# Kernel optimization log

Measured on AMD Instinct MI355X. Metric: run time of the kernel, lower is better.

Reference implementation:

```python
import jax, jax.numpy as jnp
import numpy as np

N = 20000
E = 320000
NODE_DIM = 9
EDGE_DIM = 4
HID = 64
EHID = 32  # hidden_dim // 2, edge feature dim inside GAT layers
HEADS = 4
OUT_DIM = 256
NUM_LAYERS = 3


def layer_norm(x, g, b, eps=1e-5):
    m = jnp.mean(x, axis=-1, keepdims=True)
    v = jnp.mean((x - m) ** 2, axis=-1, keepdims=True)
    return (x - m) / jnp.sqrt(v + eps) * g + b


def setup_inputs():
    key = jax.random.key(0)
    ks = iter(jax.random.split(key, 48))
    def w(shape, scale=0.1):
        return jax.random.normal(next(ks), shape, dtype=jnp.float32) * scale
    inp = {
        "x": jax.random.normal(next(ks), (N, NODE_DIM), dtype=jnp.float32),
        "edge_attr": jax.random.normal(next(ks), (E, EDGE_DIM), dtype=jnp.float32),
        "edge_index": jax.random.randint(next(ks), (2, E), 0, N, dtype=jnp.int32),
        # node encoder: Linear(9,32)+ReLU+Linear(32,64)+LayerNorm(64)
        "ne_w1": w((NODE_DIM, 32)), "ne_b1": jnp.zeros((32,), jnp.float32),
        "ne_w2": w((32, HID)), "ne_b2": jnp.zeros((HID,), jnp.float32),
        "ne_g": jnp.ones((HID,), jnp.float32), "ne_beta": jnp.zeros((HID,), jnp.float32),
        # edge encoder: Linear(4,16)+ReLU+Linear(16,32)+LayerNorm(32)
        "ee_w1": w((EDGE_DIM, 16)), "ee_b1": jnp.zeros((16,), jnp.float32),
        "ee_w2": w((16, EHID)), "ee_b2": jnp.zeros((EHID,), jnp.float32),
        "ee_g": jnp.ones((EHID,), jnp.float32), "ee_beta": jnp.zeros((EHID,), jnp.float32),
        # risk attention: Linear(96,64)+Tanh+Linear(64,1)+Sigmoid
        "ra_w1": w((HID + EHID, HID)), "ra_b1": jnp.zeros((HID,), jnp.float32),
        "ra_w2": w((HID, 1)), "ra_b2": jnp.zeros((1,), jnp.float32),
        # GAT layers (stacked over NUM_LAYERS; identical shapes)
        "gat_wl": w((NUM_LAYERS, HID, HEADS * HID)),       # linear (no bias)
        "gat_wa": w((NUM_LAYERS, 2 * HID + EHID)),          # attention (out=1, no bias)
        "gat_we": w((NUM_LAYERS, EHID, HEADS * HID)),       # edge_transform (no bias)
        "gat_wo": w((NUM_LAYERS, HID, HID)),                # output_transform weight
        "gat_wob": jnp.zeros((NUM_LAYERS, HID), jnp.float32),
        # output layer: Linear(64,128)+ReLU+Linear(128,256)+LayerNorm(256)
        "ow_1": w((HID, 128)), "ob_1": jnp.zeros((128,), jnp.float32),
        "ow_2": w((128, OUT_DIM)), "ob_2": jnp.zeros((OUT_DIM,), jnp.float32),
        "o_g": jnp.ones((OUT_DIM,), jnp.float32), "o_beta": jnp.zeros((OUT_DIM,), jnp.float32),
    }
    return inp


def reference(x, edge_attr, edge_index,
              ne_w1, ne_b1, ne_w2, ne_b2, ne_g, ne_beta,
              ee_w1, ee_b1, ee_w2, ee_b2, ee_g, ee_beta,
              ra_w1, ra_b1, ra_w2, ra_b2,
              gat_wl, gat_wa, gat_we, gat_wo, gat_wob,
              ow_1, ob_1, ow_2, ob_2, o_g, o_beta):
    row, col = edge_index[0], edge_index[1]
    # encoders
    h = layer_norm(jax.nn.relu(x @ ne_w1 + ne_b1) @ ne_w2 + ne_b2, ne_g, ne_beta)            # [N, 64]
    ef = layer_norm(jax.nn.relu(edge_attr @ ee_w1 + ee_b1) @ ee_w2 + ee_b2, ee_g, ee_beta)   # [E, 32]
    # risk weights per edge
    ri = jnp.concatenate([h[row], ef], axis=1)                                                # [E, 96]
    rw = jax.nn.sigmoid(jnp.tanh(ri @ ra_w1 + ra_b1) @ ra_w2 + ra_b2)                         # [E, 1]
    xh = h
    for l in range(NUM_LAYERS):
        xproj = (xh @ gat_wl[l]).reshape(N, HEADS, HID)                                       # [N, H, 64]
        emsg = (ef @ gat_we[l]).reshape(E, HEADS, HID)                                        # [E, H, 64]
        # attention Linear(2*64+32 -> 1) split into three slices; avoids materializing the
        # [E, H, 160] concat. Same math: cat([x_i, x_j, ef]) @ wa.
        wa_i = gat_wa[l][:HID]
        wa_j = gat_wa[l][HID:2 * HID]
        wa_e = gat_wa[l][2 * HID:]
        x_j = xproj[col]                                                                      # [E, H, 64]
        alpha = xproj[row] @ wa_i + x_j @ wa_j + (ef @ wa_e)[:, None]                         # [E, H]
        alpha = jnp.where(alpha >= 0, alpha, 0.2 * alpha)  # leaky_relu(0.2)
        alpha = alpha * rw                                  # risk modulation (broadcast [E,1])
        alpha = jax.nn.softmax(alpha, axis=0)               # softmax over ALL edges per head (as in torch code)
        agg = jax.ops.segment_sum(alpha[:, :, None] * (x_j + emsg), col, num_segments=N)      # [N, H, 64]
        xh = jax.nn.relu(agg.mean(axis=1) @ gat_wo[l] + gat_wob[l])                           # [N, 64]
    out = layer_norm(jax.nn.relu(xh @ ow_1 + ob_1) @ ow_2 + ob_2, o_g, o_beta)                # [N, 256]
    return out
```

## Files before the change

kernel.cpp:

```cpp
#include <hip/hip_runtime.h>
#include <math.h>

#define NN 20000
#define EE 320000
#define HID 64
#define EHID 32
#define HEADS 4

__device__ __forceinline__ float fast_tanh(float x) {
  float e = __expf(2.f * x);
  return 1.f - 2.f * __builtin_amdgcn_rcpf(e + 1.f);
}
__device__ __forceinline__ float fast_sigmoid(float x) {
  return __builtin_amdgcn_rcpf(1.f + __expf(-x));
}
__device__ __forceinline__ float bcast8(float v, int q) {
  switch (q) {
    case 0: return __int_as_float(__builtin_amdgcn_ds_swizzle(__float_as_int(v), (0 << 5) | 0x18));
    case 1: return __int_as_float(__builtin_amdgcn_ds_swizzle(__float_as_int(v), (1 << 5) | 0x18));
    case 2: return __int_as_float(__builtin_amdgcn_ds_swizzle(__float_as_int(v), (2 << 5) | 0x18));
    case 3: return __int_as_float(__builtin_amdgcn_ds_swizzle(__float_as_int(v), (3 << 5) | 0x18));
    case 4: return __int_as_float(__builtin_amdgcn_ds_swizzle(__float_as_int(v), (4 << 5) | 0x18));
    case 5: return __int_as_float(__builtin_amdgcn_ds_swizzle(__float_as_int(v), (5 << 5) | 0x18));
    case 6: return __int_as_float(__builtin_amdgcn_ds_swizzle(__float_as_int(v), (6 << 5) | 0x18));
    default: return __int_as_float(__builtin_amdgcn_ds_swizzle(__float_as_int(v), (7 << 5) | 0x18));
  }
}

__global__ __launch_bounds__(256) void k_node_enc(
    const float* __restrict__ x, const float* __restrict__ w1, const float* __restrict__ b1,
    const float* __restrict__ w2, const float* __restrict__ b2,
    const float* __restrict__ g, const float* __restrict__ beta,
    float* __restrict__ h) {
  int n = blockIdx.x * blockDim.x + threadIdx.x;
  if (n >= NN) return;
  float xin[9];
#pragma unroll
  for (int k = 0; k < 9; k++) xin[k] = x[n * 9 + k];
  float hid[32];
#pragma unroll
  for (int j = 0; j < 32; j++) {
    float a = b1[j];
#pragma unroll
    for (int k = 0; k < 9; k++) a += xin[k] * w1[k * 32 + j];
    hid[j] = fmaxf(a, 0.f);
  }
  float o[64];
  float s = 0.f;
  for (int j = 0; j < 64; j++) {
    float a = b2[j];
#pragma unroll
    for (int k = 0; k < 32; k++) a += hid[k] * w2[k * 64 + j];
    o[j] = a;
    s += a;
  }
  float m = s * (1.f / 64.f);
  float v = 0.f;
  for (int j = 0; j < 64; j++) { float d = o[j] - m; v += d * d; }
  v *= (1.f / 64.f);
  float inv = rsqrtf(v + 1e-5f);
#pragma unroll
  for (int j4 = 0; j4 < 16; j4++) {
    float4 r;
    r.x = (o[j4 * 4 + 0] - m) * inv * g[j4 * 4 + 0] + beta[j4 * 4 + 0];
    r.y = (o[j4 * 4 + 1] - m) * inv * g[j4 * 4 + 1] + beta[j4 * 4 + 1];
    r.z = (o[j4 * 4 + 2] - m) * inv * g[j4 * 4 + 2] + beta[j4 * 4 + 2];
    r.w = (o[j4 * 4 + 3] - m) * inv * g[j4 * 4 + 3] + beta[j4 * 4 + 3];
    ((float4*)&h[n * 64])[j4] = r;
  }
}

__global__ __launch_bounds__(256) void k_hist(const int* __restrict__ ei, int* __restrict__ counts) {
  int e = blockIdx.x * 256 + threadIdx.x;
  if (e < EE) atomicAdd(&counts[ei[EE + e]], 1);
}
__global__ __launch_bounds__(1024) void k_scan(
    const int* __restrict__ counts, int* __restrict__ rowptr, int* __restrict__ cursor) {
  __shared__ int wsum[16];
  int t = threadIdx.x, lane = t & 63, w = t >> 6;
  const int CH = 20;
  int base_i = t * CH;
  int local = 0;
  for (int i = 0; i < CH; i++) {
    int idx = base_i + i;
    if (idx < NN) local += counts[idx];
  }
  int v = local;
#pragma unroll
  for (int off = 1; off < 64; off <<= 1) {
    int u = __shfl_up(v, off);
    if (lane >= off) v += u;
  }
  if (lane == 63) wsum[w] = v;
  __syncthreads();
  int wbase = 0;
  for (int i = 0; i < w; i++) wbase += wsum[i];
  int run = wbase + v - local;
  for (int i = 0; i < CH; i++) {
    int idx = base_i + i;
    if (idx < NN) {
      rowptr[idx] = run;
      cursor[idx] = run;
      run += counts[idx];
    }
  }
  if (t == 1023) rowptr[NN] = EE;
}

__global__ __launch_bounds__(256) void k_edge_enc(
    const float* __restrict__ ea, const float* __restrict__ w1, const float* __restrict__ b1,
    const float* __restrict__ w2, const float* __restrict__ b2,
    const float* __restrict__ g, const float* __restrict__ beta,
    const float* __restrict__ gat_wa, const int* __restrict__ ei,
    int* __restrict__ cursor,
    float* __restrict__ efs, float4* __restrict__ devs4, int2* __restrict__ rcs) {
  int e = blockIdx.x * blockDim.x + threadIdx.x;
  if (e >= EE) return;
  int row = ei[e], col = ei[EE + e];
  int pos = atomicAdd(&cursor[col], 1);
  float4 xin = ((const float4*)ea)[e];
  float hid[16];
#pragma unroll
  for (int j = 0; j < 16; j++) {
    float a = b1[j];
    a += xin.x * w1[0 * 16 + j];
    a += xin.y * w1[1 * 16 + j];
    a += xin.z * w1[2 * 16 + j];
    a += xin.w * w1[3 * 16 + j];
    hid[j] = fmaxf(a, 0.f);
  }
  float o[32];
  float s = 0.f;
#pragma unroll
  for (int j = 0; j < 32; j++) {
    float a = b2[j];
#pragma unroll
    for (int k = 0; k < 16; k++) a += hid[k] * w2[k * 32 + j];
    o[j] = a;
    s += a;
  }
  float m = s * (1.f / 32.f);
  float v = 0.f;
#pragma unroll
  for (int j = 0; j < 32; j++) { float d = o[j] - m; v += d * d; }
  v *= (1.f / 32.f);
  float inv = rsqrtf(v + 1e-5f);
  float d0 = 0.f, d1 = 0.f, d2 = 0.f;
  float vn[32];
#pragma unroll
  for (int j = 0; j < 32; j++) {
    vn[j] = (o[j] - m) * inv * g[j] + beta[j];
    d0 += vn[j] * gat_wa[0 * 160 + 128 + j];
    d1 += vn[j] * gat_wa[1 * 160 + 128 + j];
    d2 += vn[j] * gat_wa[2 * 160 + 128 + j];
  }
#pragma unroll
  for (int j4 = 0; j4 < 8; j4++) {
    float4 r;
    r.x = vn[j4 * 4 + 0]; r.y = vn[j4 * 4 + 1]; r.z = vn[j4 * 4 + 2]; r.w = vn[j4 * 4 + 3];
    ((float4*)&efs[(size_t)pos * 32])[j4] = r;
  }
  devs4[pos] = make_float4(d0, d1, d2, 0.f);
  rcs[pos] = make_int2(row, col);
}

__global__ __launch_bounds__(256) void k_risk_node(
    const float* __restrict__ h, const float* __restrict__ w1, const float* __restrict__ b1,
    float* __restrict__ hnode) {
  __shared__ float xsT[64][20];
  int t = threadIdx.x;
  int n0 = blockIdx.x * 16;
  const float4* h4 = (const float4*)h;
  {
    int m = t & 15, k4 = t >> 4;
    float4 xv = h4[(n0 + m) * 16 + k4];
    xsT[k4 * 4 + 0][m] = xv.x;
    xsT[k4 * 4 + 1][m] = xv.y;
    xsT[k4 * 4 + 2][m] = xv.z;
    xsT[k4 * 4 + 3][m] = xv.w;
  }
  __syncthreads();
  int j = t & 63, grp = t >> 6;
  float bv = b1[j];
  float a0 = bv, a1 = bv, a2 = bv, a3 = bv;
  for (int k = 0; k < 64; k++) {
    float wv = w1[k * 64 + j];
    float4 xv = *(const float4*)&xsT[k][grp * 4];
    a0 += xv.x * wv; a1 += xv.y * wv; a2 += xv.z * wv; a3 += xv.w * wv;
  }
  hnode[(n0 + grp * 4 + 0) * 64 + j] = a0;
  hnode[(n0 + grp * 4 + 1) * 64 + j] = a1;
  hnode[(n0 + grp * 4 + 2) * 64 + j] = a2;
  hnode[(n0 + grp * 4 + 3) * 64 + j] = a3;
}

__global__ __launch_bounds__(256) void k_risk_edge(
    const float* __restrict__ hnode, const float* __restrict__ efs, const int2* __restrict__ rcs,
    const float* __restrict__ w1e, const float* __restrict__ w2, const float* __restrict__ b2_,
    float* __restrict__ rws) {
  int t = threadIdx.x, lane = t & 63;
  int s = lane & 7;
  int p = blockIdx.x * 256 + t;
  int myrow = rcs[p].x;
  const float4* hnode4 = (const float4*)hnode;
  const float4* efs4 = (const float4*)efs;
  const float4* w1e4 = (const float4*)w1e;
  const float4* w24 = (const float4*)w2;
  float ev[32];
#pragma unroll
  for (int i = 0; i < 8; i++) {
    float4 tmp = efs4[(size_t)p * 8 + i];
    ev[i * 4 + 0] = tmp.x; ev[i * 4 + 1] = tmp.y; ev[i * 4 + 2] = tmp.z; ev[i * 4 + 3] = tmp.w;
  }
  int rowq[8];
#pragma unroll
  for (int q = 0; q < 8; q++)
    rowq[q] = __float_as_int(bcast8(__int_as_float(myrow), q));
  float acc[8][8];
#pragma unroll
  for (int q = 0; q < 8; q++) {
    float4 ha = hnode4[(size_t)rowq[q] * 16 + s * 2];
    float4 hb = hnode4[(size_t)rowq[q] * 16 + s * 2 + 1];
    acc[q][0] = ha.x; acc[q][1] = ha.y; acc[q][2] = ha.z; acc[q][3] = ha.w;
    acc[q][4] = hb.x; acc[q][5] = hb.y; acc[q][6] = hb.z; acc[q][7] = hb.w;
  }
#pragma unroll
  for (int k = 0; k < 32; k++) {
    float4 wa4 = w1e4[k * 16 + s * 2];
    float4 wb4 = w1e4[k * 16 + s * 2 + 1];
#pragma unroll
    for (int q = 0; q < 8; q++) {
      float ekq = bcast8(ev[k], q);
      acc[q][0] += ekq * wa4.x; acc[q][1] += ekq * wa4.y;
      acc[q][2] += ekq * wa4.z; acc[q][3] += ekq * wa4.w;
      acc[q][4] += ekq * wb4.x; acc[q][5] += ekq * wb4.y;
      acc[q][6] += ekq * wb4.z; acc[q][7] += ekq * wb4.w;
    }
  }
  float4 wva = w24[s * 2], wvb = w24[s * 2 + 1];
  float tq[8];
#pragma unroll
  for (int q = 0; q < 8; q++) {
    tq[q] = fast_tanh(acc[q][0]) * wva.x + fast_tanh(acc[q][1]) * wva.y +
            fast_tanh(acc[q][2]) * wva.z + fast_tanh(acc[q][3]) * wva.w +
            fast_tanh(acc[q][4]) * wvb.x + fast_tanh(acc[q][5]) * wvb.y +
            fast_tanh(acc[q][6]) * wvb.z + fast_tanh(acc[q][7]) * wvb.w;
  }
#pragma unroll
  for (int q = 0; q < 8; q++) {
    tq[q] += __shfl_xor(tq[q], 1);
    tq[q] += __shfl_xor(tq[q], 2);
    tq[q] += __shfl_xor(tq[q], 4);
  }
  float mine = tq[0];
  mine = (s == 1) ? tq[1] : mine;
  mine = (s == 2) ? tq[2] : mine;
  mine = (s == 3) ? tq[3] : mine;
  mine = (s == 4) ? tq[4] : mine;
  mine = (s == 5) ? tq[5] : mine;
  mine = (s == 6) ? tq[6] : mine;
  mine = (s == 7) ? tq[7] : mine;
  rws[p] = fast_sigmoid(mine + b2_[0]);
}

__global__ __launch_bounds__(256) void k_xproj(
    const float* __restrict__ xh, const float* __restrict__ wl, const float* __restrict__ wa,
    float* __restrict__ xproj, float* __restrict__ di, float* __restrict__ dj) {
  __shared__ float xsT[64][20];
  int t = threadIdx.x, lane = t & 63, w = t >> 6;
  int n0 = blockIdx.x * 16;
  const float4* xh4 = (const float4*)xh;
  {
    int m = t & 15, k4 = t >> 4;
    float4 xv = xh4[(n0 + m) * 16 + k4];
    xsT[k4 * 4 + 0][m] = xv.x;
    xsT[k4 * 4 + 1][m] = xv.y;
    xsT[k4 * 4 + 2][m] = xv.z;
    xsT[k4 * 4 + 3][m] = xv.w;
  }
  __syncthreads();
  float acc[16];
#pragma unroll
  for (int m = 0; m < 16; m++) acc[m] = 0.f;
  for (int k = 0; k < 64; k++) {
    float wv = wl[k * 256 + t];
    float4 xa = *(const float4*)&xsT[k][0];
    float4 xb = *(const float4*)&xsT[k][4];
    float4 xc = *(const float4*)&xsT[k][8];
    float4 xd = *(const float4*)&xsT[k][12];
    acc[0] += xa.x * wv; acc[1] += xa.y * wv; acc[2] += xa.z * wv; acc[3] += xa.w * wv;
    acc[4] += xb.x * wv; acc[5] += xb.y * wv; acc[6] += xb.z * wv; acc[7] += xb.w * wv;
    acc[8] += xc.x * wv; acc[9] += xc.y * wv; acc[10] += xc.z * wv; acc[11] += xc.w * wv;
    acc[12] += xd.x * wv; acc[13] += xd.y * wv; acc[14] += xd.z * wv; acc[15] += xd.w * wv;
  }
  float wai = wa[lane], waj = wa[64 + lane];
#pragma unroll
  for (int m = 0; m < 16; m++) {
    xproj[(n0 + m) * 256 + t] = acc[m];
    float vi = acc[m] * wai;
    float vj = acc[m] * waj;
#pragma unroll
    for (int off = 32; off; off >>= 1) { vi += __shfl_xor(vi, off); vj += __shfl_xor(vj, off); }
    if (lane == 0) { di[(n0 + m) * 4 + w] = vi; dj[(n0 + m) * 4 + w] = vj; }
  }
}

__global__ __launch_bounds__(256) void k_pexp(
    const int2* __restrict__ rcs, const float4* __restrict__ devs4,
    const float* __restrict__ rws, const float* __restrict__ di,
    const float* __restrict__ dj, int layer,
    float4* __restrict__ ps4, float* __restrict__ gsum_l) {
  __shared__ float wred[4][4];
  int t = threadIdx.x, lane = t & 63, w = t >> 6;
  int i = blockIdx.x * 256 + t;
  int2 rc = rcs[i];
  float4 dv = devs4[i];
  float dev = (layer == 0) ? dv.x : ((layer == 1) ? dv.y : dv.z);
  float rv = rws[i];
  float4 dr = ((const float4*)di)[rc.x];
  float4 djc = ((const float4*)dj)[rc.y];
  float z0 = dr.x + djc.x + dev, z1 = dr.y + djc.y + dev;
  float z2 = dr.z + djc.z + dev, z3 = dr.w + djc.w + dev;
  z0 = ((z0 >= 0.f) ? z0 : 0.2f * z0) * rv;
  z1 = ((z1 >= 0.f) ? z1 : 0.2f * z1) * rv;
  z2 = ((z2 >= 0.f) ? z2 : 0.2f * z2) * rv;
  z3 = ((z3 >= 0.f) ? z3 : 0.2f * z3) * rv;
  float4 pv;
  pv.x = __expf(z0); pv.y = __expf(z1); pv.z = __expf(z2); pv.w = __expf(z3);
  ps4[i] = pv;
  float sh[4] = {pv.x, pv.y, pv.z, pv.w};
#pragma unroll
  for (int h = 0; h < 4; h++) {
    float v = sh[h];
#pragma unroll
    for (int off = 32; off; off >>= 1) v += __shfl_xor(v, off);
    if (lane == 0) wred[w][h] = v;
  }
  __syncthreads();
  if (t < 4) atomicAdd(&gsum_l[t], wred[0][t] + wred[1][t] + wred[2][t] + wred[3][t]);
}

__global__ __launch_bounds__(256) void k_agg(
    const int* __restrict__ rowptr, const float4* __restrict__ ps4,
    const float* __restrict__ efs,
    float* __restrict__ sagg, float* __restrict__ tagg) {
  int t = threadIdx.x, lane = t & 63, wv = t >> 6;
  int n = blockIdx.x * 4 + wv;
  int c = lane & 31, slot = lane >> 5;
  float a0 = 0.f, a1 = 0.f, a2 = 0.f, a3 = 0.f;
  float s0 = 0.f, s1 = 0.f, s2 = 0.f, s3 = 0.f;
  int beg = rowptr[n], end = rowptr[n + 1];
  int i = beg + slot;
  for (; i + 2 < end; i += 4) {
    float4 pa = ps4[i];
    float eva = efs[(size_t)i * 32 + c];
    float4 pb = ps4[i + 2];
    float evb = efs[(size_t)(i + 2) * 32 + c];
    a0 += pa.x * eva + pb.x * evb;
    a1 += pa.y * eva + pb.y * evb;
    a2 += pa.z * eva + pb.z * evb;
    a3 += pa.w * eva + pb.w * evb;
    s0 += pa.x + pb.x; s1 += pa.y + pb.y;
    s2 += pa.z + pb.z; s3 += pa.w + pb.w;
  }
  if (i < end) {
    float4 pa = ps4[i];
    float eva = efs[(size_t)i * 32 + c];
    a0 += pa.x * eva; a1 += pa.y * eva; a2 += pa.z * eva; a3 += pa.w * eva;
    s0 += pa.x; s1 += pa.y; s2 += pa.z; s3 += pa.w;
  }
  a0 += __shfl_xor(a0, 32); a1 += __shfl_xor(a1, 32);
  a2 += __shfl_xor(a2, 32); a3 += __shfl_xor(a3, 32);
  s0 += __shfl_xor(s0, 32); s1 += __shfl_xor(s1, 32);
  s2 += __shfl_xor(s2, 32); s3 += __shfl_xor(s3, 32);
  if (slot == 0) {
    tagg[n * 128 + 0 * 32 + c] = a0;
    tagg[n * 128 + 1 * 32 + c] = a1;
    tagg[n * 128 + 2 * 32 + c] = a2;
    tagg[n * 128 + 3 * 32 + c] = a3;
    if (c < 4) {
      float sv = (c == 0) ? s0 : (c == 1) ? s1 : (c == 2) ? s2 : s3;
      sagg[n * 4 + c] = sv;
    }
  }
}

template <bool DO_XPROJ>
__global__ __launch_bounds__(256) void k_update_fused(
    const float* __restrict__ xproj, const float* __restrict__ sagg,
    const float* __restrict__ tagg, const float* __restrict__ gsum_l,
    const float* __restrict__ we, const float* __restrict__ wo, const float* __restrict__ wob,
    const float* __restrict__ wl_next, const float* __restrict__ wa_next,
    float* __restrict__ xh_out, float* __restrict__ xproj_out,
    float* __restrict__ di, float* __restrict__ dj) {
  __shared__ float tsT[128][20];
  __shared__ float usT[64][20];
  __shared__ float xhT[64][20];
  __shared__ float ss[16][4];
  int t = threadIdx.x, lane = t & 63, w = t >> 6;
  int n0 = blockIdx.x * 16;
  float4 gs = *((const float4*)gsum_l);
  float inv0 = 1.0f / gs.x, inv1 = 1.0f / gs.y, inv2 = 1.0f / gs.z, inv3 = 1.0f / gs.w;
  const float4* tagg4 = (const float4*)tagg;
  for (int i = t; i < 16 * 32; i += 256) {
    int m = i & 15, k4 = i >> 4;
    float invh = (k4 < 8) ? inv0 : (k4 < 16) ? inv1 : (k4 < 24) ? inv2 : inv3;
    float4 tv = tagg4[(n0 + m) * 32 + k4];
    tsT[k4 * 4 + 0][m] = tv.x * invh;
    tsT[k4 * 4 + 1][m] = tv.y * invh;
    tsT[k4 * 4 + 2][m] = tv.z * invh;
    tsT[k4 * 4 + 3][m] = tv.w * invh;
  }
  if (t < 64) {
    int hh = t & 3;
    float invh = (hh == 0) ? inv0 : (hh == 1) ? inv1 : (hh == 2) ? inv2 : inv3;
    ss[t >> 2][hh] = sagg[n0 * 4 + t] * invh;
  }
  __syncthreads();
  int j = lane, grp = w;
  float u0 = 0.f, u1 = 0.f, u2 = 0.f, u3 = 0.f;
#pragma unroll
  for (int h = 0; h < 4; h++) {
    u0 += xproj[(n0 + grp * 4 + 0) * 256 + h * 64 + j] * ss[grp * 4 + 0][h];
    u1 += xproj[(n0 + grp * 4 + 1) * 256 + h * 64 + j] * ss[grp * 4 + 1][h];
    u2 += xproj[(n0 + grp * 4 + 2) * 256 + h * 64 + j] * ss[grp * 4 + 2][h];
    u3 += xproj[(n0 + grp * 4 + 3) * 256 + h * 64 + j] * ss[grp * 4 + 3][h];
  }
  for (int hc = 0; hc < 128; hc++) {
    float wv = we[(hc & 31) * 256 + (hc >> 5) * 64 + j];
    float4 tv = *(const float4*)&tsT[hc][grp * 4];
    u0 += tv.x * wv; u1 += tv.y * wv; u2 += tv.z * wv; u3 += tv.w * wv;
  }
  *(float4*)&usT[j][grp * 4] = make_float4(u0 * 0.25f, u1 * 0.25f, u2 * 0.25f, u3 * 0.25f);
  __syncthreads();
  float ob = wob[j];
  float o0 = ob, o1 = ob, o2 = ob, o3 = ob;
  for (int k = 0; k < 64; k++) {
    float wv = wo[k * 64 + j];
    float4 uv = *(const float4*)&usT[k][grp * 4];
    o0 += uv.x * wv; o1 += uv.y * wv; o2 += uv.z * wv; o3 += uv.w * wv;
  }
  o0 = fmaxf(o0, 0.f); o1 = fmaxf(o1, 0.f); o2 = fmaxf(o2, 0.f); o3 = fmaxf(o3, 0.f);
  if (!DO_XPROJ) {
    xh_out[(n0 + grp * 4 + 0) * 64 + j] = o0;
    xh_out[(n0 + grp * 4 + 1) * 64 + j] = o1;
    xh_out[(n0 + grp * 4 + 2) * 64 + j] = o2;
    xh_out[(n0 + grp * 4 + 3) * 64 + j] = o3;
    return;
  }
  xhT[j][grp * 4 + 0] = o0;
  xhT[j][grp * 4 + 1] = o1;
  xhT[j][grp * 4 + 2] = o2;
  xhT[j][grp * 4 + 3] = o3;
  __syncthreads();
  float acc[16];
#pragma unroll
  for (int m = 0; m < 16; m++) acc[m] = 0.f;
  for (int k = 0; k < 64; k++) {
    float wv = wl_next[k * 256 + t];
    float4 xa = *(const float4*)&xhT[k][0];
    float4 xb = *(const float4*)&xhT[k][4];
    float4 xc = *(const float4*)&xhT[k][8];
    float4 xd = *(const float4*)&xhT[k][12];
    acc[0] += xa.x * wv; acc[1] += xa.y * wv; acc[2] += xa.z * wv; acc[3] += xa.w * wv;
    acc[4] += xb.x * wv; acc[5] += xb.y * wv; acc[6] += xb.z * wv; acc[7] += xb.w * wv;
    acc[8] += xc.x * wv; acc[9] += xc.y * wv; acc[10] += xc.z * wv; acc[11] += xc.w * wv;
    acc[12] += xd.x * wv; acc[13] += xd.y * wv; acc[14] += xd.z * wv; acc[15] += xd.w * wv;
  }
  float wai = wa_next[lane], waj = wa_next[64 + lane];
#pragma unroll
  for (int m = 0; m < 16; m++) {
    xproj_out[(n0 + m) * 256 + t] = acc[m];
    float vi = acc[m] * wai;
    float vj = acc[m] * waj;
#pragma unroll
    for (int off = 32; off; off >>= 1) { vi += __shfl_xor(vi, off); vj += __shfl_xor(vj, off); }
    if (lane == 0) { di[(n0 + m) * 4 + w] = vi; dj[(n0 + m) * 4 + w] = vj; }
  }
}

#define OPN 8
__global__ __launch_bounds__(256) void k_out(
    const float* __restrict__ xh, const float* __restrict__ w1, const float* __restrict__ b1,
    const float* __restrict__ w2, const float* __restrict__ b2,
    const float* __restrict__ g, const float* __restrict__ beta,
    float* __restrict__ out) {
  __shared__ float xsT[64][12];
  __shared__ float hsT[128][12];
  __shared__ float wp[4], wq[4];
  int t = threadIdx.x, lane = t & 63, w = t >> 6;
  int n0 = blockIdx.x * OPN;
  const float4* xh4 = (const float4*)xh;
  if (t < 128) {
    int m = t >> 4, k4 = t & 15;
    float4 xv = xh4[(n0 + m) * 16 + k4];
    xsT[k4 * 4 + 0][m] = xv.x;
    xsT[k4 * 4 + 1][m] = xv.y;
    xsT[k4 * 4 + 2][m] = xv.z;
    xsT[k4 * 4 + 3][m] = xv.w;
  }
  __syncthreads();
  for (int i = t; i < OPN * 128; i += 256) {
    int m = i >> 7, jj = i & 127;
    float a = b1[jj];
#pragma unroll
    for (int k = 0; k < 64; k++) a += xsT[k][m] * w1[k * 128 + jj];
    hsT[jj][m] = fmaxf(a, 0.f);
  }
  __syncthreads();
  float o[OPN];
  float bb = b2[t];
#pragma unroll
  for (int m = 0; m < OPN; m++) o[m] = bb;
  for (int k = 0; k < 128; k++) {
    float wv = w2[k * 256 + t];
    float4 ha = *(const float4*)&hsT[k][0];
    float4 hb = *(const float4*)&hsT[k][4];
    o[0] += ha.x * wv; o[1] += ha.y * wv; o[2] += ha.z * wv; o[3] += ha.w * wv;
    o[4] += hb.x * wv; o[5] += hb.y * wv; o[6] += hb.z * wv; o[7] += hb.w * wv;
  }
  float gv = g[t], bv = beta[t];
#pragma unroll
  for (int m = 0; m < OPN; m++) {
    float v = o[m], vv = o[m] * o[m];
#pragma unroll
    for (int off = 32; off; off >>= 1) { v += __shfl_xor(v, off); vv += __shfl_xor(vv, off); }
    if (lane == 0) { wp[w] = v; wq[w] = vv; }
    __syncthreads();
    float mean = (wp[0] + wp[1] + wp[2] + wp[3]) * (1.f / 256.f);
    float ex2 = (wq[0] + wq[1] + wq[2] + wq[3]) * (1.f / 256.f);
    float var = ex2 - mean * mean;
    __syncthreads();
    out[(n0 + m) * 256 + t] = (o[m] - mean) * rsqrtf(var + 1e-5f) * gv + bv;
  }
}

extern "C" void kernel_launch(void* const* d_in, const int* in_sizes, int n_in,
                              void* d_out, int out_size, void* d_ws, size_t ws_size,
                              hipStream_t stream) {
  const float* x         = (const float*)d_in[0];
  const float* edge_attr = (const float*)d_in[1];
  const int*   ei        = (const int*)d_in[2];
  const float* ne_w1 = (const float*)d_in[3];
  const float* ne_b1 = (const float*)d_in[4];
  const float* ne_w2 = (const float*)d_in[5];
  const float* ne_b2 = (const float*)d_in[6];
  const float* ne_g  = (const float*)d_in[7];
  const float* ne_be = (const float*)d_in[8];
  const float* ee_w1 = (const float*)d_in[9];
  const float* ee_b1 = (const float*)d_in[10];
  const float* ee_w2 = (const float*)d_in[11];
  const float* ee_b2 = (const float*)d_in[12];
  const float* ee_g  = (const float*)d_in[13];
  const float* ee_be = (const float*)d_in[14];
  const float* ra_w1 = (const float*)d_in[15];
  const float* ra_b1 = (const float*)d_in[16];
  const float* ra_w2 = (const float*)d_in[17];
  const float* ra_b2 = (const float*)d_in[18];
  const float* gat_wl  = (const float*)d_in[19];
  const float* gat_wa  = (const float*)d_in[20];
  const float* gat_we  = (const float*)d_in[21];
  const float* gat_wo  = (const float*)d_in[22];
  const float* gat_wob = (const float*)d_in[23];
  const float* ow_1 = (const float*)d_in[24];
  const float* ob_1 = (const float*)d_in[25];
  const float* ow_2 = (const float*)d_in[26];
  const float* ob_2 = (const float*)d_in[27];
  const float* o_g  = (const float*)d_in[28];
  const float* o_be = (const float*)d_in[29];
  float* out = (float*)d_out;

  char* wsb = (char*)d_ws;
  size_t off = 0;
  auto af = [&](size_t elems) -> float* { float* p = (float*)(wsb + off); off += elems * sizeof(float); return p; };
  auto ai = [&](size_t elems) -> int*   { int*   p = (int*)(wsb + off);   off += elems * sizeof(int);   return p; };

  float* h      = af((size_t)NN * 64);
  float* xh2    = af((size_t)NN * 64);
  float* efs    = af((size_t)EE * 32);
  float* devs   = af((size_t)EE * 4);
  float* rws    = af((size_t)EE);
  float* ps     = af((size_t)EE * 4);
  float* xprojA = af((size_t)NN * 256);
  float* xprojB = af((size_t)NN * 256);
  float* di     = af((size_t)NN * 4);
  float* dj     = af((size_t)NN * 4);
  float* sagg   = af((size_t)NN * 4);
  float* tagg   = af((size_t)NN * 128);
  float* gsum   = af(12);
  int* rcs    = ai(2 * (size_t)EE);
  int* counts = ai(NN);
  int* rowptr = ai(NN + 1);
  int* cursor = ai(NN);
  float* hnode = xprojB;
  (void)ws_size; (void)n_in; (void)in_sizes; (void)out_size;

  hipMemsetAsync(counts, 0, NN * sizeof(int), stream);
  hipMemsetAsync(gsum, 0, 12 * sizeof(float), stream);
  k_hist<<<EE / 256, 256, 0, stream>>>(ei, counts);
  k_node_enc<<<(NN + 255) / 256, 256, 0, stream>>>(x, ne_w1, ne_b1, ne_w2, ne_b2, ne_g, ne_be, h);
  k_scan<<<1, 1024, 0, stream>>>(counts, rowptr, cursor);
  k_edge_enc<<<EE / 256, 256, 0, stream>>>(edge_attr, ee_w1, ee_b1, ee_w2, ee_b2, ee_g, ee_be,
                                           gat_wa, ei, cursor, efs, (float4*)devs, (int2*)rcs);
  k_risk_node<<<NN / 16, 256, 0, stream>>>(h, ra_w1, ra_b1, hnode);
  k_risk_edge<<<EE / 256, 256, 0, stream>>>(hnode, efs, (const int2*)rcs,
                                            ra_w1 + 64 * 64, ra_w2, ra_b2, rws);
  k_xproj<<<NN / 16, 256, 0, stream>>>(h, gat_wl, gat_wa, xprojA, di, dj);

  float* xp_cur = xprojA;
  float* xp_nxt = xprojB;
  for (int l = 0; l < 3; l++) {
    const float* we  = gat_we + (size_t)l * 32 * 256;
    const float* wo  = gat_wo + (size_t)l * 64 * 64;
    const float* wob = gat_wob + (size_t)l * 64;
    float* gsum_l = gsum + l * 4;

    k_pexp<<<EE / 256, 256, 0, stream>>>((const int2*)rcs, (const float4*)devs, rws,
                                         di, dj, l, (float4*)ps, gsum_l);
    k_agg<<<NN / 4, 256, 0, stream>>>(rowptr, (const float4*)ps, efs, sagg, tagg);
    if (l < 2) {
      const float* wl_n = gat_wl + (size_t)(l + 1) * 64 * 256;
      const float* wa_n = gat_wa + (size_t)(l + 1) * 160;
      k_update_fused<true><<<NN / 16, 256, 0, stream>>>(
          xp_cur, sagg, tagg, gsum_l, we, wo, wob, wl_n, wa_n, nullptr, xp_nxt, di, dj);
      float* tmp = xp_cur; xp_cur = xp_nxt; xp_nxt = tmp;
    } else {
      k_update_fused<false><<<NN / 16, 256, 0, stream>>>(
          xp_cur, sagg, tagg, gsum_l, we, wo, wob, nullptr, nullptr, xh2, nullptr, nullptr, nullptr);
    }
  }

  k_out<<<NN / OPN, 256, 0, stream>>>(xh2, ow_1, ob_1, ow_2, ob_2, o_g, o_be, out);
}
```

Baseline: 546.7 us.

## Fuse edge aggregation into node update kernel and widen output-layer node tile

Merges the per-node edge aggregation into the update kernel, so each block aggregates its 16 nodes' incoming edges straight into shared memory instead of writing and re-reading the tagg/sagg buffers. This saves a kernel launch per layer and a global round trip of the aggregated features. In exchange the aggregation now runs with fewer blocks (NN/16 rather than NN/4), and each wave walks 4 nodes serially, which may lower memory-level parallelism. Separately, the output kernel processes 16 nodes per block instead of 8 and does its LayerNorm reductions in one batch with a single barrier instead of two barriers per node.

Result: faster. 531.1 us (-2.9%).

```diff
diff --git a/kernel.cpp b/kernel.cpp
--- a/kernel.cpp
+++ b/kernel.cpp
@@ -340,55 +340,11 @@
   if (t < 4) atomicAdd(&gsum_l[t], wred[0][t] + wred[1][t] + wred[2][t] + wred[3][t]);
 }
 
-__global__ __launch_bounds__(256) void k_agg(
+template <bool DO_XPROJ>
+__global__ __launch_bounds__(256) void k_aggupdate(
     const int* __restrict__ rowptr, const float4* __restrict__ ps4,
-    const float* __restrict__ efs,
-    float* __restrict__ sagg, float* __restrict__ tagg) {
-  int t = threadIdx.x, lane = t & 63, wv = t >> 6;
-  int n = blockIdx.x * 4 + wv;
-  int c = lane & 31, slot = lane >> 5;
-  float a0 = 0.f, a1 = 0.f, a2 = 0.f, a3 = 0.f;
-  float s0 = 0.f, s1 = 0.f, s2 = 0.f, s3 = 0.f;
-  int beg = rowptr[n], end = rowptr[n + 1];
-  int i = beg + slot;
-  for (; i + 2 < end; i += 4) {
-    float4 pa = ps4[i];
-    float eva = efs[(size_t)i * 32 + c];
-    float4 pb = ps4[i + 2];
-    float evb = efs[(size_t)(i + 2) * 32 + c];
-    a0 += pa.x * eva + pb.x * evb;
-    a1 += pa.y * eva + pb.y * evb;
-    a2 += pa.z * eva + pb.z * evb;
-    a3 += pa.w * eva + pb.w * evb;
-    s0 += pa.x + pb.x; s1 += pa.y + pb.y;
-    s2 += pa.z + pb.z; s3 += pa.w + pb.w;
-  }
-  if (i < end) {
-    float4 pa = ps4[i];
-    float eva = efs[(size_t)i * 32 + c];
-    a0 += pa.x * eva; a1 += pa.y * eva; a2 += pa.z * eva; a3 += pa.w * eva;
-    s0 += pa.x; s1 += pa.y; s2 += pa.z; s3 += pa.w;
-  }
-  a0 += __shfl_xor(a0, 32); a1 += __shfl_xor(a1, 32);
-  a2 += __shfl_xor(a2, 32); a3 += __shfl_xor(a3, 32);
-  s0 += __shfl_xor(s0, 32); s1 += __shfl_xor(s1, 32);
-  s2 += __shfl_xor(s2, 32); s3 += __shfl_xor(s3, 32);
-  if (slot == 0) {
-    tagg[n * 128 + 0 * 32 + c] = a0;
-    tagg[n * 128 + 1 * 32 + c] = a1;
-    tagg[n * 128 + 2 * 32 + c] = a2;
-    tagg[n * 128 + 3 * 32 + c] = a3;
-    if (c < 4) {
-      float sv = (c == 0) ? s0 : (c == 1) ? s1 : (c == 2) ? s2 : s3;
-      sagg[n * 4 + c] = sv;
-    }
-  }
-}
-
-template <bool DO_XPROJ>
-__global__ __launch_bounds__(256) void k_update_fused(
-    const float* __restrict__ xproj, const float* __restrict__ sagg,
-    const float* __restrict__ tagg, const float* __restrict__ gsum_l,
+    const float* __restrict__ efs, const float* __restrict__ gsum_l,
+    const float* __restrict__ xproj,
     const float* __restrict__ we, const float* __restrict__ wo, const float* __restrict__ wob,
     const float* __restrict__ wl_next, const float* __restrict__ wa_next,
     float* __restrict__ xh_out, float* __restrict__ xproj_out,
@@ -397,27 +353,55 @@
   __shared__ float usT[64][20];
   __shared__ float xhT[64][20];
   __shared__ float ss[16][4];
-  int t = threadIdx.x, lane = t & 63, w = t >> 6;
+  int t = threadIdx.x, lane = t & 63, wv = t >> 6;
   int n0 = blockIdx.x * 16;
   float4 gs = *((const float4*)gsum_l);
   float inv0 = 1.0f / gs.x, inv1 = 1.0f / gs.y, inv2 = 1.0f / gs.z, inv3 = 1.0f / gs.w;
-  const float4* tagg4 = (const float4*)tagg;
-  for (int i = t; i < 16 * 32; i += 256) {
-    int m = i & 15, k4 = i >> 4;
-    float invh = (k4 < 8) ? inv0 : (k4 < 16) ? inv1 : (k4 < 24) ? inv2 : inv3;
-    float4 tv = tagg4[(n0 + m) * 32 + k4];
-    tsT[k4 * 4 + 0][m] = tv.x * invh;
-    tsT[k4 * 4 + 1][m] = tv.y * invh;
-    tsT[k4 * 4 + 2][m] = tv.z * invh;
-    tsT[k4 * 4 + 3][m] = tv.w * invh;
-  }
-  if (t < 64) {
-    int hh = t & 3;
-    float invh = (hh == 0) ? inv0 : (hh == 1) ? inv1 : (hh == 2) ? inv2 : inv3;
-    ss[t >> 2][hh] = sagg[n0 * 4 + t] * invh;
-  }
-  __syncthreads();
-  int j = lane, grp = w;
+  int c = lane & 31, slot = lane >> 5;
+#pragma unroll
+  for (int q = 0; q < 4; q++) {
+    int n = n0 + wv * 4 + q;
+    int beg = rowptr[n], end = rowptr[n + 1];
+    float a0 = 0.f, a1 = 0.f, a2 = 0.f, a3 = 0.f;
+    float s0 = 0.f, s1 = 0.f, s2 = 0.f, s3 = 0.f;
+    int i = beg + slot;
+    for (; i + 2 < end; i += 4) {
+      float4 pa = ps4[i];
+      float eva = efs[(size_t)i * 32 + c];
+      float4 pb = ps4[i + 2];
+      float evb = efs[(size_t)(i + 2) * 32 + c];
+      a0 += pa.x * eva + pb.x * evb;
+      a1 += pa.y * eva + pb.y * evb;
+      a2 += pa.z * eva + pb.z * evb;
+      a3 += pa.w * eva + pb.w * evb;
+      s0 += pa.x + pb.x; s1 += pa.y + pb.y;
+      s2 += pa.z + pb.z; s3 += pa.w + pb.w;
+    }
+    if (i < end) {
+      float4 pa = ps4[i];
+      float eva = efs[(size_t)i * 32 + c];
+      a0 += pa.x * eva; a1 += pa.y * eva; a2 += pa.z * eva; a3 += pa.w * eva;
+      s0 += pa.x; s1 += pa.y; s2 += pa.z; s3 += pa.w;
+    }
+    a0 += __shfl_xor(a0, 32); a1 += __shfl_xor(a1, 32);
+    a2 += __shfl_xor(a2, 32); a3 += __shfl_xor(a3, 32);
+    s0 += __shfl_xor(s0, 32); s1 += __shfl_xor(s1, 32);
+    s2 += __shfl_xor(s2, 32); s3 += __shfl_xor(s3, 32);
+    if (slot == 0) {
+      int m = wv * 4 + q;
+      tsT[0 * 32 + c][m] = a0 * inv0;
+      tsT[1 * 32 + c][m] = a1 * inv1;
+      tsT[2 * 32 + c][m] = a2 * inv2;
+      tsT[3 * 32 + c][m] = a3 * inv3;
+      if (c < 4) {
+        float sv = (c == 0) ? s0 : (c == 1) ? s1 : (c == 2) ? s2 : s3;
+        float iv = (c == 0) ? inv0 : (c == 1) ? inv1 : (c == 2) ? inv2 : inv3;
+        ss[m][c] = sv * iv;
+      }
+    }
+  }
+  __syncthreads();
+  int j = lane, grp = wv;
   float u0 = 0.f, u1 = 0.f, u2 = 0.f, u3 = 0.f;
 #pragma unroll
   for (int h = 0; h < 4; h++) {
@@ -427,18 +411,18 @@
     u3 += xproj[(n0 + grp * 4 + 3) * 256 + h * 64 + j] * ss[grp * 4 + 3][h];
   }
   for (int hc = 0; hc < 128; hc++) {
-    float wv = we[(hc & 31) * 256 + (hc >> 5) * 64 + j];
+    float wv2 = we[(hc & 31) * 256 + (hc >> 5) * 64 + j];
     float4 tv = *(const float4*)&tsT[hc][grp * 4];
-    u0 += tv.x * wv; u1 += tv.y * wv; u2 += tv.z * wv; u3 += tv.w * wv;
+    u0 += tv.x * wv2; u1 += tv.y * wv2; u2 += tv.z * wv2; u3 += tv.w * wv2;
   }
   *(float4*)&usT[j][grp * 4] = make_float4(u0 * 0.25f, u1 * 0.25f, u2 * 0.25f, u3 * 0.25f);
   __syncthreads();
   float ob = wob[j];
   float o0 = ob, o1 = ob, o2 = ob, o3 = ob;
   for (int k = 0; k < 64; k++) {
-    float wv = wo[k * 64 + j];
+    float wv2 = wo[k * 64 + j];
     float4 uv = *(const float4*)&usT[k][grp * 4];
-    o0 += uv.x * wv; o1 += uv.y * wv; o2 += uv.z * wv; o3 += uv.w * wv;
+    o0 += uv.x * wv2; o1 += uv.y * wv2; o2 += uv.z * wv2; o3 += uv.w * wv2;
   }
   o0 = fmaxf(o0, 0.f); o1 = fmaxf(o1, 0.f); o2 = fmaxf(o2, 0.f); o3 = fmaxf(o3, 0.f);
   if (!DO_XPROJ) {
@@ -457,15 +441,15 @@
 #pragma unroll
   for (int m = 0; m < 16; m++) acc[m] = 0.f;
   for (int k = 0; k < 64; k++) {
-    float wv = wl_next[k * 256 + t];
+    float wv2 = wl_next[k * 256 + t];
     float4 xa = *(const float4*)&xhT[k][0];
     float4 xb = *(const float4*)&xhT[k][4];
     float4 xc = *(const float4*)&xhT[k][8];
     float4 xd = *(const float4*)&xhT[k][12];
-    acc[0] += xa.x * wv; acc[1] += xa.y * wv; acc[2] += xa.z * wv; acc[3] += xa.w * wv;
-    acc[4] += xb.x * wv; acc[5] += xb.y * wv; acc[6] += xb.z * wv; acc[7] += xb.w * wv;
-    acc[8] += xc.x * wv; acc[9] += xc.y * wv; acc[10] += xc.z * wv; acc[11] += xc.w * wv;
-    acc[12] += xd.x * wv; acc[13] += xd.y * wv; acc[14] += xd.z * wv; acc[15] += xd.w * wv;
+    acc[0] += xa.x * wv2; acc[1] += xa.y * wv2; acc[2] += xa.z * wv2; acc[3] += xa.w * wv2;
+    acc[4] += xb.x * wv2; acc[5] += xb.y * wv2; acc[6] += xb.z * wv2; acc[7] += xb.w * wv2;
+    acc[8] += xc.x * wv2; acc[9] += xc.y * wv2; acc[10] += xc.z * wv2; acc[11] += xc.w * wv2;
+    acc[12] += xd.x * wv2; acc[13] += xd.y * wv2; acc[14] += xd.z * wv2; acc[15] += xd.w * wv2;
   }
   float wai = wa_next[lane], waj = wa_next[64 + lane];
 #pragma unroll
@@ -475,24 +459,24 @@
     float vj = acc[m] * waj;
 #pragma unroll
     for (int off = 32; off; off >>= 1) { vi += __shfl_xor(vi, off); vj += __shfl_xor(vj, off); }
-    if (lane == 0) { di[(n0 + m) * 4 + w] = vi; dj[(n0 + m) * 4 + w] = vj; }
-  }
-}
-
-#define OPN 8
+    if (lane == 0) { di[(n0 + m) * 4 + wv] = vi; dj[(n0 + m) * 4 + wv] = vj; }
+  }
+}
+
+#define OPN 16
 __global__ __launch_bounds__(256) void k_out(
     const float* __restrict__ xh, const float* __restrict__ w1, const float* __restrict__ b1,
     const float* __restrict__ w2, const float* __restrict__ b2,
     const float* __restrict__ g, const float* __restrict__ beta,
     float* __restrict__ out) {
-  __shared__ float xsT[64][12];
-  __shared__ float hsT[128][12];
-  __shared__ float wp[4], wq[4];
+  __shared__ float xsT[64][17];
+  __shared__ float hsT[128][20];
+  __shared__ float wp[16][4], wq[16][4];
   int t = threadIdx.x, lane = t & 63, w = t >> 6;
   int n0 = blockIdx.x * OPN;
   const float4* xh4 = (const float4*)xh;
-  if (t < 128) {
-    int m = t >> 4, k4 = t & 15;
+  {
+    int m = t & 15, k4 = t >> 4;
     float4 xv = xh4[(n0 + m) * 16 + k4];
     xsT[k4 * 4 + 0][m] = xv.x;
     xsT[k4 * 4 + 1][m] = xv.y;
@@ -514,23 +498,29 @@
   for (int m = 0; m < OPN; m++) o[m] = bb;
   for (int k = 0; k < 128; k++) {
     float wv = w2[k * 256 + t];
-    float4 ha = *(const float4*)&hsT[k][0];
-    float4 hb = *(const float4*)&hsT[k][4];
-    o[0] += ha.x * wv; o[1] += ha.y * wv; o[2] += ha.z * wv; o[3] += ha.w * wv;
-    o[4] += hb.x * wv; o[5] += hb.y * wv; o[6] += hb.z * wv; o[7] += hb.w * wv;
-  }
-  float gv = g[t], bv = beta[t];
+    float4 h0 = *(const float4*)&hsT[k][0];
+    float4 h1 = *(const float4*)&hsT[k][4];
+    float4 h2 = *(const float4*)&hsT[k][8];
+    float4 h3 = *(const float4*)&hsT[k][12];
+    o[0] += h0.x * wv; o[1] += h0.y * wv; o[2] += h0.z * wv; o[3] += h0.w * wv;
+    o[4] += h1.x * wv; o[5] += h1.y * wv; o[6] += h1.z * wv; o[7] += h1.w * wv;
+    o[8] += h2.x * wv; o[9] += h2.y * wv; o[10] += h2.z * wv; o[11] += h2.w * wv;
+    o[12] += h3.x * wv; o[13] += h3.y * wv; o[14] += h3.z * wv; o[15] += h3.w * wv;
+  }
 #pragma unroll
   for (int m = 0; m < OPN; m++) {
     float v = o[m], vv = o[m] * o[m];
 #pragma unroll
     for (int off = 32; off; off >>= 1) { v += __shfl_xor(v, off); vv += __shfl_xor(vv, off); }
-    if (lane == 0) { wp[w] = v; wq[w] = vv; }
-    __syncthreads();
-    float mean = (wp[0] + wp[1] + wp[2] + wp[3]) * (1.f / 256.f);
-    float ex2 = (wq[0] + wq[1] + wq[2] + wq[3]) * (1.f / 256.f);
+    if (lane == 0) { wp[m][w] = v; wq[m][w] = vv; }
+  }
+  __syncthreads();
+  float gv = g[t], bv = beta[t];
+#pragma unroll
+  for (int m = 0; m < OPN; m++) {
+    float mean = (wp[m][0] + wp[m][1] + wp[m][2] + wp[m][3]) * (1.f / 256.f);
+    float ex2 = (wq[m][0] + wq[m][1] + wq[m][2] + wq[m][3]) * (1.f / 256.f);
     float var = ex2 - mean * mean;
-    __syncthreads();
     out[(n0 + m) * 256 + t] = (o[m] - mean) * rsqrtf(var + 1e-5f) * gv + bv;
   }
 }
@@ -585,8 +575,6 @@
   float* xprojB = af((size_t)NN * 256);
   float* di     = af((size_t)NN * 4);
   float* dj     = af((size_t)NN * 4);
-  float* sagg   = af((size_t)NN * 4);
-  float* tagg   = af((size_t)NN * 128);
   float* gsum   = af(12);
   int* rcs    = ai(2 * (size_t)EE);
   int* counts = ai(NN);
@@ -617,16 +605,17 @@
 
     k_pexp<<<EE / 256, 256, 0, stream>>>((const int2*)rcs, (const float4*)devs, rws,
                                          di, dj, l, (float4*)ps, gsum_l);
-    k_agg<<<NN / 4, 256, 0, stream>>>(rowptr, (const float4*)ps, efs, sagg, tagg);
     if (l < 2) {
       const float* wl_n = gat_wl + (size_t)(l + 1) * 64 * 256;
       const float* wa_n = gat_wa + (size_t)(l + 1) * 160;
-      k_update_fused<true><<<NN / 16, 256, 0, stream>>>(
-          xp_cur, sagg, tagg, gsum_l, we, wo, wob, wl_n, wa_n, nullptr, xp_nxt, di, dj);
+      k_aggupdate<true><<<NN / 16, 256, 0, stream>>>(
+          rowptr, (const float4*)ps, efs, gsum_l, xp_cur, we, wo, wob, wl_n, wa_n,
+          nullptr, xp_nxt, di, dj);
       float* tmp = xp_cur; xp_cur = xp_nxt; xp_nxt = tmp;
     } else {
-      k_update_fused<false><<<NN / 16, 256, 0, stream>>>(
-          xp_cur, sagg, tagg, gsum_l, we, wo, wob, nullptr, nullptr, xh2, nullptr, nullptr, nullptr);
+      k_aggupdate<false><<<NN / 16, 256, 0, stream>>>(
+          rowptr, (const float4*)ps, efs, gsum_l, xp_cur, we, wo, wob, nullptr, nullptr,
+          xh2, nullptr, nullptr, nullptr);
     }
   }
 
```
